# Optimization experiments

Hardware: AMD Instinct MI355X
Metric: run time of the kernel (lower is better)

Reference implementation:

```python
import jax, jax.numpy as jnp
import numpy as np

V, G, F, T = 500000, 25000, 256, 2


def setup_inputs() -> dict:
    key = jax.random.key(0)
    ks = jax.random.split(key, 10)
    s = 1.0 / np.sqrt(F)
    node_feats = jax.random.normal(ks[0], (V, F), jnp.float32)
    seg_ids = jnp.sort(jax.random.randint(ks[1], (V,), 0, G, dtype=jnp.int32))
    Wl = jax.random.uniform(ks[2], (T, 1, 2 * F), jnp.float32, -s, s)
    bl = jax.random.uniform(ks[3], (T, 1), jnp.float32, -s, s)
    Wp = jax.random.uniform(ks[4], (T, F, F), jnp.float32, -s, s)
    bp = jax.random.uniform(ks[5], (T, F), jnp.float32, -s, s)
    Wih = jax.random.uniform(ks[6], (T, 3 * F, F), jnp.float32, -s, s)
    Whh = jax.random.uniform(ks[7], (T, 3 * F, F), jnp.float32, -s, s)
    bih = jax.random.uniform(ks[8], (T, 3 * F), jnp.float32, -s, s)
    bhh = jax.random.uniform(ks[9], (T, 3 * F), jnp.float32, -s, s)
    return dict(node_feats=node_feats, seg_ids=seg_ids, Wl=Wl, bl=bl,
                Wp=Wp, bp=bp, Wih=Wih, Whh=Whh, bih=bih, bhh=bhh)


def _segment_softmax(z, seg):
    # z: (V,) per-node logits; softmax within each graph segment
    m = jax.ops.segment_max(z, seg, num_segments=G)
    m = jnp.where(jnp.isfinite(m), m, 0.0)  # guard empty segments
    e = jnp.exp(z - m[seg])
    d = jax.ops.segment_sum(e, seg, num_segments=G)
    return e / d[seg]


def _gru_cell(x, h, Wih, Whh, bih, bhh):
    # torch.nn.GRUCell semantics
    gi = x @ Wih.T + bih  # (G, 3F)
    gh = h @ Whh.T + bhh
    ir, iz, inn = jnp.split(gi, 3, axis=1)
    hr, hz, hn = jnp.split(gh, 3, axis=1)
    r = jax.nn.sigmoid(ir + hr)
    zg = jax.nn.sigmoid(iz + hz)
    n = jnp.tanh(inn + r * hn)
    return (1.0 - zg) * n + zg * h


def reference(node_feats, seg_ids, Wl, bl, Wp, bp, Wih, Whh, bih, bhh):
    # initial graph feats = sum of node feats per graph
    g_feats = jax.ops.segment_sum(node_feats, seg_ids, num_segments=G)  # (G, F)
    for t in range(T):
        ctx_in = jnp.concatenate([jax.nn.relu(g_feats)[seg_ids], node_feats], axis=1)  # (V, 2F)
        z = jax.nn.leaky_relu(ctx_in @ Wl[t].T + bl[t], 0.01)[:, 0]  # (V,)
        a = _segment_softmax(z, seg_ids)[:, None]  # (V, 1)
        hv = node_feats @ Wp[t].T + bp[t]  # dropout=0 -> identity
        g_repr = jax.ops.segment_sum(a * hv, seg_ids, num_segments=G)  # (G, F)
        context = jax.nn.elu(g_repr)
        g_feats = _gru_cell(context, g_feats, Wih[t], Whh[t], bih[t], bhh[t])
    return g_feats
```

## Files before the change

### kernel.cpp

```cpp
#include <hip/hip_runtime.h>
#include <cstdint>

typedef unsigned short u16;
typedef unsigned int u32;

#define V_N 500000
#define G_N 25000
#define F_N 256
#define GP_N 25088
#define CAP 64

typedef __attribute__((ext_vector_type(8))) __bf16 bf16x8;
typedef __attribute__((ext_vector_type(4))) float f32x4;

__device__ __forceinline__ u16 f2bf(float f) {
  u32 u = __builtin_bit_cast(u32, f);
  u += 0x7fffu + ((u >> 16) & 1u);
  return (u16)(u >> 16);
}
__device__ __forceinline__ float bf2f(u16 s) {
  u32 u = ((u32)s) << 16;
  return __builtin_bit_cast(float, u);
}
__device__ __forceinline__ float sigm(float x) { return 1.f / (1.f + __expf(-x)); }
__device__ __forceinline__ float tanh_fast(float x) {
  return 1.f - 2.f / (__expf(2.f * x) + 1.f);
}

__device__ __forceinline__ void load_lds16(const void* g, void* l) {
  __builtin_amdgcn_global_load_lds(
      (const __attribute__((address_space(1))) void*)g,
      (__attribute__((address_space(3))) void*)l, 16, 0, 0);
}

__global__ __launch_bounds__(256) void k_convw(const float* __restrict__ Wp,
                                               const float* __restrict__ Wih,
                                               const float* __restrict__ Whh,
                                               u16* __restrict__ Wpb, u16* __restrict__ W3) {
  int i = blockIdx.x * 256 + threadIdx.x;
  const int NP = 2 * F_N * F_N;
  if (i < NP) {
    Wpb[i] = f2bf(Wp[i]);
    return;
  }
  int j = i - NP;
  int t = j >> 19;
  int r = j & 524287;
  int row = r >> 9;
  int k = r & 511;
  int q = row >> 6;
  int gate = (row >> 4) & 3;
  int c = q * 16 + (row & 15);
  const float* wi = Wih + t * 196608;
  const float* wh = Whh + t * 196608;
  float v;
  if (gate == 0) {
    v = (k < 256) ? wi[c * 256 + k] : wh[c * 256 + (k - 256)];
  } else if (gate == 1) {
    v = (k < 256) ? wi[(256 + c) * 256 + k] : wh[(256 + c) * 256 + (k - 256)];
  } else if (gate == 2) {
    v = (k < 256) ? wi[(512 + c) * 256 + k] : 0.f;
  } else {
    v = (k >= 256) ? wh[(512 + c) * 256 + (k - 256)] : 0.f;
  }
  W3[j] = f2bf(v);
}

__global__ __launch_bounds__(256) void k_offsets(const int* __restrict__ seg, int* __restrict__ off) {
  int v = blockIdx.x * 256 + threadIdx.x;
  if (v > V_N) return;
  if (v == 0) {
    int c = seg[0];
    for (int g = 0; g <= c; ++g) off[g] = 0;
  } else if (v == V_N) {
    int pr = seg[V_N - 1];
    for (int g = pr + 1; g <= G_N; ++g) off[g] = V_N;
  } else {
    int pr = seg[v - 1], c = seg[v];
    for (int g = pr + 1; g <= c; ++g) off[g] = v;
  }
}

__device__ __forceinline__ float blk_sum(float v, float* lds4) {
#pragma unroll
  for (int m = 32; m >= 1; m >>= 1) v += __shfl_xor(v, m, 64);
  __syncthreads();
  if ((threadIdx.x & 63) == 0) lds4[threadIdx.x >> 6] = v;
  __syncthreads();
  return lds4[0] + lds4[1] + lds4[2] + lds4[3];
}
__device__ __forceinline__ float blk_max(float v, float* lds4) {
#pragma unroll
  for (int m = 32; m >= 1; m >>= 1) v = fmaxf(v, __shfl_xor(v, m, 64));
  __syncthreads();
  if ((threadIdx.x & 63) == 0) lds4[threadIdx.x >> 6] = v;
  __syncthreads();
  return fmaxf(fmaxf(lds4[0], lds4[1]), fmaxf(lds4[2], lds4[3]));
}

template <int USEXB>
__global__ __launch_bounds__(256) void k_node_fused(const float* __restrict__ nf,
                                                    const int* __restrict__ off,
                                                    const float* __restrict__ Wl,
                                                    const float* __restrict__ bl,
                                                    u16* __restrict__ xb,
                                                    float* __restrict__ q0, float* __restrict__ q1,
                                                    float* __restrict__ hbuf0, u16* __restrict__ x2a,
                                                    u16* __restrict__ x2b,
                                                    u16* __restrict__ sb, float* __restrict__ Ag) {
  int g = blockIdx.x;
  int tid = threadIdx.x, lane = tid & 63, w = tid >> 6;
  if (g >= G_N) {
    hbuf0[(size_t)g * F_N + tid] = 0.f;
    x2a[(size_t)g * 512 + 256 + tid] = 0;
    x2b[(size_t)g * 512 + 256 + tid] = 0;
    sb[(size_t)g * F_N + tid] = 0;
    if (tid == 0) Ag[g] = 0.f;
    return;
  }
  __shared__ __align__(16) u16 xcache[CAP * F_N];
  __shared__ float zrow[CAP];
  __shared__ float red[4][256];
  __shared__ float a_s[256];
  __shared__ float lds4[4];

  float w0[4], w1[4];
#pragma unroll
  for (int j = 0; j < 4; ++j) {
    w0[j] = Wl[256 + lane * 4 + j];
    w1[j] = Wl[512 + 256 + lane * 4 + j];
  }
  int s = off[g], e = off[g + 1];
  int n = e - s;
  float a0 = 0.f, a1 = 0.f, a2 = 0.f, a3 = 0.f;
  for (int v = s + w; v < e; v += 4) {
    const float4 x = *reinterpret_cast<const float4*>(nf + (size_t)v * F_N + lane * 4);
    a0 += x.x; a1 += x.y; a2 += x.z; a3 += x.w;
    uint2 pk;
    pk.x = (u32)f2bf(x.x) | ((u32)f2bf(x.y) << 16);
    pk.y = (u32)f2bf(x.z) | ((u32)f2bf(x.w) << 16);
    if (USEXB) *reinterpret_cast<uint2*>(xb + (size_t)v * F_N + lane * 4) = pk;
    int li = v - s;
    if (li < CAP) *reinterpret_cast<uint2*>(&xcache[li * F_N + lane * 4]) = pk;
    float d0 = x.x * w0[0] + x.y * w0[1] + x.z * w0[2] + x.w * w0[3];
    float d1 = x.x * w1[0] + x.y * w1[1] + x.z * w1[2] + x.w * w1[3];
#pragma unroll
    for (int m = 32; m >= 1; m >>= 1) {
      d0 += __shfl_xor(d0, m, 64);
      d1 += __shfl_xor(d1, m, 64);
    }
    if (lane == 0) {
      q0[v] = d0;
      q1[v] = d1;
      if (li < CAP) zrow[li] = d0;
    }
  }
  red[w][lane * 4 + 0] = a0;
  red[w][lane * 4 + 1] = a1;
  red[w][lane * 4 + 2] = a2;
  red[w][lane * 4 + 3] = a3;
  __threadfence_block();
  __syncthreads();
  float sval = red[0][tid] + red[1][tid] + red[2][tid] + red[3][tid];
  hbuf0[(size_t)g * F_N + tid] = sval;
  x2a[(size_t)g * 512 + 256 + tid] = f2bf(sval);

  float p = blk_sum(fmaxf(sval, 0.f) * Wl[tid], lds4) + bl[0];
  if (n == 0) {
    sb[(size_t)g * F_N + tid] = 0;
    if (tid == 0) Ag[g] = 0.f;
    return;
  }
  float mloc = -3.4e38f;
  for (int i = tid; i < n; i += 256) {
    float zq = (i < CAP) ? zrow[i] : q0[s + i];
    float z = p + zq;
    z = z >= 0.f ? z : 0.01f * z;
    mloc = fmaxf(mloc, z);
  }
  float mx = blk_max(mloc, lds4);
  float dloc = 0.f;
  for (int i = tid; i < n; i += 256) {
    float zq = (i < CAP) ? zrow[i] : q0[s + i];
    float z = p + zq;
    z = z >= 0.f ? z : 0.01f * z;
    dloc += __expf(z - mx);
  }
  float inv = 1.f / blk_sum(dloc, lds4);

  float acc4[4] = {0.f, 0.f, 0.f, 0.f};
  for (int c0 = 0; c0 < n; c0 += 256) {
    int cnt = min(256, n - c0);
    __syncthreads();
    if (tid < cnt) {
      int i = c0 + tid;
      float zq = (i < CAP) ? zrow[i] : q0[s + i];
      float z = p + zq;
      z = z >= 0.f ? z : 0.01f * z;
      a_s[tid] = __expf(z - mx) * inv;
    }
    __syncthreads();
    for (int j = w; j < cnt; j += 4) {
      int i = c0 + j;
      float a = a_s[j];
      uint2 u;
      if (i < CAP) {
        u = *reinterpret_cast<const uint2*>(&xcache[i * F_N + lane * 4]);
      } else if (USEXB) {
        u = *reinterpret_cast<const uint2*>(xb + (size_t)(s + i) * F_N + lane * 4);
      } else {
        float4 x = *reinterpret_cast<const float4*>(nf + (size_t)(s + i) * F_N + lane * 4);
        acc4[0] += a * x.x; acc4[1] += a * x.y; acc4[2] += a * x.z; acc4[3] += a * x.w;
        continue;
      }
      acc4[0] += a * bf2f((u16)(u.x & 0xffff));
      acc4[1] += a * bf2f((u16)(u.x >> 16));
      acc4[2] += a * bf2f((u16)(u.y & 0xffff));
      acc4[3] += a * bf2f((u16)(u.y >> 16));
    }
  }
  __syncthreads();
  red[w][lane * 4 + 0] = acc4[0];
  red[w][lane * 4 + 1] = acc4[1];
  red[w][lane * 4 + 2] = acc4[2];
  red[w][lane * 4 + 3] = acc4[3];
  __syncthreads();
  float sv = red[0][tid] + red[1][tid] + red[2][tid] + red[3][tid];
  sb[(size_t)g * F_N + tid] = f2bf(sv);
  if (tid == 0) Ag[g] = 1.f;
}

template <int USEXB>
__global__ __launch_bounds__(256) void k_attn(const float* __restrict__ h,
                                              const u16* __restrict__ xb, const float* __restrict__ nf,
                                              const float* __restrict__ q, const int* __restrict__ off,
                                              const float* __restrict__ Wl, const float* __restrict__ bl,
                                              int t, u16* __restrict__ sb, float* __restrict__ Ag) {
  int g = blockIdx.x;
  int tid = threadIdx.x, lane = tid & 63, w = tid >> 6;
  __shared__ float lds4[4];
  __shared__ float a_s[256];
  __shared__ float red[4][256];

  float hv = fmaxf(h[(size_t)g * F_N + tid], 0.f);
  float p = blk_sum(hv * Wl[t * 512 + tid], lds4) + bl[t];

  int s = off[g], n = off[g + 1] - s;
  if (n == 0) {
    sb[(size_t)g * F_N + tid] = 0;
    if (tid == 0) Ag[g] = 0.f;
    return;
  }
  float mloc = -3.4e38f;
  for (int i = tid; i < n; i += 256) {
    float z = p + q[s + i];
    z = z >= 0.f ? z : 0.01f * z;
    mloc = fmaxf(mloc, z);
  }
  float mx = blk_max(mloc, lds4);
  float dloc = 0.f;
  for (int i = tid; i < n; i += 256) {
    float z = p + q[s + i];
    z = z >= 0.f ? z : 0.01f * z;
    dloc += __expf(z - mx);
  }
  float inv = 1.f / blk_sum(dloc, lds4);

  float acc[4] = {0.f, 0.f, 0.f, 0.f};
  for (int c0 = 0; c0 < n; c0 += 256) {
    int cnt = min(256, n - c0);
    __syncthreads();
    if (tid < cnt) {
      float z = p + q[s + c0 + tid];
      z = z >= 0.f ? z : 0.01f * z;
      a_s[tid] = __expf(z - mx) * inv;
    }
    __syncthreads();
    for (int j = w; j < cnt; j += 4) {
      float a = a_s[j];
      size_t base = (size_t)(s + c0 + j) * F_N + lane * 4;
      if (USEXB) {
        uint2 u = *reinterpret_cast<const uint2*>(xb + base);
        acc[0] += a * bf2f((u16)(u.x & 0xffff));
        acc[1] += a * bf2f((u16)(u.x >> 16));
        acc[2] += a * bf2f((u16)(u.y & 0xffff));
        acc[3] += a * bf2f((u16)(u.y >> 16));
      } else {
        float4 x = *reinterpret_cast<const float4*>(nf + base);
        acc[0] += a * x.x; acc[1] += a * x.y; acc[2] += a * x.z; acc[3] += a * x.w;
      }
    }
  }
  __syncthreads();
  red[w][lane * 4 + 0] = acc[0];
  red[w][lane * 4 + 1] = acc[1];
  red[w][lane * 4 + 2] = acc[2];
  red[w][lane * 4 + 3] = acc[3];
  __syncthreads();
  float sv = red[0][tid] + red[1][tid] + red[2][tid] + red[3][tid];
  sb[(size_t)g * F_N + tid] = f2bf(sv);
  if (tid == 0) Ag[g] = 1.f;
}

__global__ __launch_bounds__(256) void k_gemm(const u16* __restrict__ A, const u16* __restrict__ B,
                                              int K, float* __restrict__ dst,
                                              u16* __restrict__ x2out, const float* __restrict__ AgH,
                                              const float* __restrict__ b1, const float* __restrict__ b2,
                                              int mode, int writehb) {
  __shared__ __align__(16) u16 As[128 * 64];
  __shared__ __align__(16) u16 Bs[128 * 64];
  int tid = threadIdx.x, lane = tid & 63, w = tid >> 6;
  int m0 = blockIdx.x * 128, n0 = blockIdx.y * 128;
  int wm = w >> 1, wn = w & 1;
  f32x4 zero = {0.f, 0.f, 0.f, 0.f};
  f32x4 acc[4][4];
#pragma unroll
  for (int i = 0; i < 4; ++i)
#pragma unroll
    for (int j = 0; j < 4; ++j) acc[i][j] = zero;

  int rowA = tid >> 3;
  int col8 = (tid & 7) * 8;
  for (int k0 = 0; k0 < K; k0 += 64) {
    __syncthreads();
#pragma unroll
    for (int c = 0; c < 4; ++c) {
      int r = c * 32 + rowA;
      const u16* gA = A + (size_t)(m0 + r) * K + k0 + col8;
      const u16* gB = B + (size_t)(n0 + r) * K + k0 + col8;
      char* lA = (char*)As + (c * 256 + w * 64) * 16;
      char* lB = (char*)Bs + (c * 256 + w * 64) * 16;
      load_lds16(gA, lA);
      load_lds16(gB, lB);
    }
    __syncthreads();
#pragma unroll
    for (int kk = 0; kk < 64; kk += 32) {
      bf16x8 af[4], bfr[4];
#pragma unroll
      for (int i = 0; i < 4; ++i) {
        af[i] = *reinterpret_cast<const bf16x8*>(&As[(wm * 64 + i * 16 + (lane & 15)) * 64 + kk + (lane >> 4) * 8]);
        bfr[i] = *reinterpret_cast<const bf16x8*>(&Bs[(wn * 64 + i * 16 + (lane & 15)) * 64 + kk + (lane >> 4) * 8]);
      }
#pragma unroll
      for (int i = 0; i < 4; ++i)
#pragma unroll
        for (int j = 0; j < 4; ++j)
          acc[i][j] = __builtin_amdgcn_mfma_f32_16x16x32_bf16(af[i], bfr[j], acc[i][j], 0, 0, 0);
    }
  }
  int crow0 = m0 + wm * 64 + (lane >> 4) * 4;
  if (mode == 1) {
    int ccol0 = n0 + wn * 64 + (lane & 15);
#pragma unroll
    for (int i = 0; i < 4; ++i)
#pragma unroll
      for (int j = 0; j < 4; ++j) {
        int col = ccol0 + j * 16;
#pragma unroll
        for (int r = 0; r < 4; ++r) {
          int row = crow0 + i * 16 + r;
          float v = acc[i][j][r] + AgH[row] * b1[col];
          v = v > 0.f ? v : (__expf(v) - 1.f);
          x2out[(size_t)row * 512 + col] = f2bf(v);
        }
      }
  } else {
    int qgrp = blockIdx.y * 2 + wn;
    int c = qgrp * 16 + (lane & 15);
    float bi0 = b1[c] + b2[c];
    float bi1 = b1[256 + c] + b2[256 + c];
    float bi2 = b1[512 + c];
    float bi3 = b2[512 + c];
#pragma unroll
    for (int i = 0; i < 4; ++i)
#pragma unroll
      for (int r = 0; r < 4; ++r) {
        int grow = crow0 + i * 16 + r;
        if (grow >= G_N) continue;
        float ir = acc[i][0][r] + bi0;
        float iz = acc[i][1][r] + bi1;
        float nn = acc[i][2][r] + bi2;
        float hn = acc[i][3][r] + bi3;
        float rg = sigm(ir);
        float zg = sigm(iz);
        float h0 = AgH[(size_t)grow * F_N + c];
        float nv = tanh_fast(nn + rg * hn);
        float hN = (1.f - zg) * nv + zg * h0;
        dst[(size_t)grow * F_N + c] = hN;
        if (writehb) x2out[(size_t)grow * 512 + 256 + c] = f2bf(hN);
      }
  }
}

extern "C" void kernel_launch(void* const* d_in, const int* in_sizes, int n_in,
                              void* d_out, int out_size, void* d_ws, size_t ws_size,
                              hipStream_t stream) {
  const float* nf = (const float*)d_in[0];
  const int* seg = (const int*)d_in[1];
  const float* Wl = (const float*)d_in[2];
  const float* bl = (const float*)d_in[3];
  const float* Wp = (const float*)d_in[4];
  const float* bp = (const float*)d_in[5];
  const float* Wih = (const float*)d_in[6];
  const float* Whh = (const float*)d_in[7];
  const float* bih = (const float*)d_in[8];
  const float* bhh = (const float*)d_in[9];
  float* out = (float*)d_out;

  char* p = (char*)d_ws;
  auto alloc = [&](size_t bytes) {
    char* r = p;
    p += (bytes + 511) & ~(size_t)511;
    return r;
  };
  float* q0 = (float*)alloc((size_t)V_N * 4);
  float* q1 = (float*)alloc((size_t)V_N * 4);
  int* off = (int*)alloc((size_t)(G_N + 1) * 4);
  float* hbuf0 = (float*)alloc((size_t)GP_N * F_N * 4);
  float* hbuf1 = (float*)alloc((size_t)GP_N * F_N * 4);
  u16* sb = (u16*)alloc((size_t)GP_N * F_N * 2);
  float* Ag = (float*)alloc((size_t)GP_N * 4);
  u16* X2a = (u16*)alloc((size_t)GP_N * 512 * 2);
  u16* X2b = (u16*)alloc((size_t)GP_N * 512 * 2);
  u16* Wpb = (u16*)alloc((size_t)2 * F_N * F_N * 2);
  u16* W3 = (u16*)alloc((size_t)2 * 1024 * 512 * 2);
  size_t fixed = (size_t)(p - (char*)d_ws);
  bool usexb = (fixed + (size_t)V_N * F_N * 2) <= ws_size;
  u16* xb = usexb ? (u16*)alloc((size_t)V_N * F_N * 2) : nullptr;

  k_convw<<<4608, 256, 0, stream>>>(Wp, Wih, Whh, Wpb, W3);
  k_offsets<<<(V_N + 1 + 255) / 256, 256, 0, stream>>>(seg, off);
  if (usexb)
    k_node_fused<1><<<GP_N, 256, 0, stream>>>(nf, off, Wl, bl, xb, q0, q1, hbuf0, X2a, X2b, sb, Ag);
  else
    k_node_fused<0><<<GP_N, 256, 0, stream>>>(nf, off, Wl, bl, xb, q0, q1, hbuf0, X2a, X2b, sb, Ag);

  k_gemm<<<dim3(GP_N / 128, 2), 256, 0, stream>>>(sb, Wpb, 256,
                                                  nullptr, X2a, Ag, bp, nullptr, 1, 0);
  k_gemm<<<dim3(GP_N / 128, 8), 256, 0, stream>>>(X2a, W3, 512,
                                                  hbuf1, X2b, hbuf0,
                                                  bih, bhh, 2, 1);
  if (usexb)
    k_attn<1><<<G_N, 256, 0, stream>>>(hbuf1, xb, nf, q1, off, Wl, bl, 1, sb, Ag);
  else
    k_attn<0><<<G_N, 256, 0, stream>>>(hbuf1, xb, nf, q1, off, Wl, bl, 1, sb, Ag);
  k_gemm<<<dim3(GP_N / 128, 2), 256, 0, stream>>>(sb, Wpb + 65536, 256,
                                                  nullptr, X2b, Ag, bp + 256, nullptr, 1, 0);
  k_gemm<<<dim3(GP_N / 128, 8), 256, 0, stream>>>(X2b, W3 + 524288, 512,
                                                  out, nullptr, hbuf1,
                                                  bih + 768, bhh + 768, 2, 0);
}
```

Measured before the change: 520.7 us.

## Map one graph per wavefront and split fused node kernel from attention

The per-graph node and attention kernels now assign one graph per 64-lane wavefront, with four graphs per block, instead of one graph per 256-thread block. This drops the LDS reductions and __syncthreads barriers. The fused node kernel is split: k_node computes sums, bf16 copies and q projections, and the first-step attention becomes a separate k_attn launch. The LDS node cache and the fp32 fallback path are removed, and the attention loop reads 16-byte bf16 rows with two rows per wavefront step. The intent is to cut synchronization overhead and raise occupancy for small segments of about 20 nodes. The cost is an extra launch, a re-read of xb for step 0, and an unconditional xb allocation that assumes the workspace is large enough.

```diff
diff --git a/kernel.cpp b/kernel.cpp
--- a/kernel.cpp
+++ b/kernel.cpp
@@ -8,7 +8,6 @@
 #define G_N 25000
 #define F_N 256
 #define GP_N 25088
-#define CAP 64
 
 typedef __attribute__((ext_vector_type(8))) __bf16 bf16x8;
 typedef __attribute__((ext_vector_type(4))) float f32x4;
@@ -26,6 +25,7 @@
 __device__ __forceinline__ float tanh_fast(float x) {
   return 1.f - 2.f / (__expf(2.f * x) + 1.f);
 }
+__device__ __forceinline__ float lrelu(float z) { return z >= 0.f ? z : 0.01f * z; }
 
 __device__ __forceinline__ void load_lds16(const void* g, void* l) {
   __builtin_amdgcn_global_load_lds(
@@ -81,69 +81,40 @@
   }
 }
 
-__device__ __forceinline__ float blk_sum(float v, float* lds4) {
-#pragma unroll
-  for (int m = 32; m >= 1; m >>= 1) v += __shfl_xor(v, m, 64);
-  __syncthreads();
-  if ((threadIdx.x & 63) == 0) lds4[threadIdx.x >> 6] = v;
-  __syncthreads();
-  return lds4[0] + lds4[1] + lds4[2] + lds4[3];
-}
-__device__ __forceinline__ float blk_max(float v, float* lds4) {
-#pragma unroll
-  for (int m = 32; m >= 1; m >>= 1) v = fmaxf(v, __shfl_xor(v, m, 64));
-  __syncthreads();
-  if ((threadIdx.x & 63) == 0) lds4[threadIdx.x >> 6] = v;
-  __syncthreads();
-  return fmaxf(fmaxf(lds4[0], lds4[1]), fmaxf(lds4[2], lds4[3]));
-}
-
-template <int USEXB>
-__global__ __launch_bounds__(256) void k_node_fused(const float* __restrict__ nf,
-                                                    const int* __restrict__ off,
-                                                    const float* __restrict__ Wl,
-                                                    const float* __restrict__ bl,
-                                                    u16* __restrict__ xb,
-                                                    float* __restrict__ q0, float* __restrict__ q1,
-                                                    float* __restrict__ hbuf0, u16* __restrict__ x2a,
-                                                    u16* __restrict__ x2b,
-                                                    u16* __restrict__ sb, float* __restrict__ Ag) {
-  int g = blockIdx.x;
-  int tid = threadIdx.x, lane = tid & 63, w = tid >> 6;
+__global__ __launch_bounds__(256) void k_node(const float* __restrict__ nf,
+                                              const int* __restrict__ off,
+                                              const float* __restrict__ Wl,
+                                              u16* __restrict__ xb,
+                                              float* __restrict__ q0, float* __restrict__ q1,
+                                              float* __restrict__ hbuf0, u16* __restrict__ x2a,
+                                              u16* __restrict__ x2b,
+                                              u16* __restrict__ sb, float* __restrict__ Ag) {
+  int g = blockIdx.x * 4 + (threadIdx.x >> 6);
+  int lane = threadIdx.x & 63;
+  if (g >= GP_N) return;
   if (g >= G_N) {
-    hbuf0[(size_t)g * F_N + tid] = 0.f;
-    x2a[(size_t)g * 512 + 256 + tid] = 0;
-    x2b[(size_t)g * 512 + 256 + tid] = 0;
-    sb[(size_t)g * F_N + tid] = 0;
-    if (tid == 0) Ag[g] = 0.f;
+    float4 z4 = {0.f, 0.f, 0.f, 0.f};
+    uint2 z2 = {0u, 0u};
+    *reinterpret_cast<float4*>(hbuf0 + (size_t)g * F_N + lane * 4) = z4;
+    *reinterpret_cast<uint2*>(x2a + (size_t)g * 512 + 256 + lane * 4) = z2;
+    *reinterpret_cast<uint2*>(x2b + (size_t)g * 512 + 256 + lane * 4) = z2;
+    *reinterpret_cast<uint2*>(sb + (size_t)g * F_N + lane * 4) = z2;
+    if (lane == 0) Ag[g] = 0.f;
     return;
   }
-  __shared__ __align__(16) u16 xcache[CAP * F_N];
-  __shared__ float zrow[CAP];
-  __shared__ float red[4][256];
-  __shared__ float a_s[256];
-  __shared__ float lds4[4];
-
-  float w0[4], w1[4];
-#pragma unroll
-  for (int j = 0; j < 4; ++j) {
-    w0[j] = Wl[256 + lane * 4 + j];
-    w1[j] = Wl[512 + 256 + lane * 4 + j];
-  }
+  const float4 w0 = *reinterpret_cast<const float4*>(Wl + 256 + lane * 4);
+  const float4 w1 = *reinterpret_cast<const float4*>(Wl + 768 + lane * 4);
   int s = off[g], e = off[g + 1];
-  int n = e - s;
   float a0 = 0.f, a1 = 0.f, a2 = 0.f, a3 = 0.f;
-  for (int v = s + w; v < e; v += 4) {
+  for (int v = s; v < e; ++v) {
     const float4 x = *reinterpret_cast<const float4*>(nf + (size_t)v * F_N + lane * 4);
     a0 += x.x; a1 += x.y; a2 += x.z; a3 += x.w;
     uint2 pk;
     pk.x = (u32)f2bf(x.x) | ((u32)f2bf(x.y) << 16);
     pk.y = (u32)f2bf(x.z) | ((u32)f2bf(x.w) << 16);
-    if (USEXB) *reinterpret_cast<uint2*>(xb + (size_t)v * F_N + lane * 4) = pk;
-    int li = v - s;
-    if (li < CAP) *reinterpret_cast<uint2*>(&xcache[li * F_N + lane * 4]) = pk;
-    float d0 = x.x * w0[0] + x.y * w0[1] + x.z * w0[2] + x.w * w0[3];
-    float d1 = x.x * w1[0] + x.y * w1[1] + x.z * w1[2] + x.w * w1[3];
+    *reinterpret_cast<uint2*>(xb + (size_t)v * F_N + lane * 4) = pk;
+    float d0 = x.x * w0.x + x.y * w0.y + x.z * w0.z + x.w * w0.w;
+    float d1 = x.x * w1.x + x.y * w1.y + x.z * w1.z + x.w * w1.w;
 #pragma unroll
     for (int m = 32; m >= 1; m >>= 1) {
       d0 += __shfl_xor(d0, m, 64);
@@ -152,154 +123,87 @@
     if (lane == 0) {
       q0[v] = d0;
       q1[v] = d1;
-      if (li < CAP) zrow[li] = d0;
-    }
-  }
-  red[w][lane * 4 + 0] = a0;
-  red[w][lane * 4 + 1] = a1;
-  red[w][lane * 4 + 2] = a2;
-  red[w][lane * 4 + 3] = a3;
-  __threadfence_block();
-  __syncthreads();
-  float sval = red[0][tid] + red[1][tid] + red[2][tid] + red[3][tid];
-  hbuf0[(size_t)g * F_N + tid] = sval;
-  x2a[(size_t)g * 512 + 256 + tid] = f2bf(sval);
-
-  float p = blk_sum(fmaxf(sval, 0.f) * Wl[tid], lds4) + bl[0];
-  if (n == 0) {
-    sb[(size_t)g * F_N + tid] = 0;
-    if (tid == 0) Ag[g] = 0.f;
-    return;
-  }
-  float mloc = -3.4e38f;
-  for (int i = tid; i < n; i += 256) {
-    float zq = (i < CAP) ? zrow[i] : q0[s + i];
-    float z = p + zq;
-    z = z >= 0.f ? z : 0.01f * z;
-    mloc = fmaxf(mloc, z);
-  }
-  float mx = blk_max(mloc, lds4);
-  float dloc = 0.f;
-  for (int i = tid; i < n; i += 256) {
-    float zq = (i < CAP) ? zrow[i] : q0[s + i];
-    float z = p + zq;
-    z = z >= 0.f ? z : 0.01f * z;
-    dloc += __expf(z - mx);
-  }
-  float inv = 1.f / blk_sum(dloc, lds4);
-
-  float acc4[4] = {0.f, 0.f, 0.f, 0.f};
-  for (int c0 = 0; c0 < n; c0 += 256) {
-    int cnt = min(256, n - c0);
-    __syncthreads();
-    if (tid < cnt) {
-      int i = c0 + tid;
-      float zq = (i < CAP) ? zrow[i] : q0[s + i];
-      float z = p + zq;
-      z = z >= 0.f ? z : 0.01f * z;
-      a_s[tid] = __expf(z - mx) * inv;
-    }
-    __syncthreads();
-    for (int j = w; j < cnt; j += 4) {
-      int i = c0 + j;
-      float a = a_s[j];
-      uint2 u;
-      if (i < CAP) {
-        u = *reinterpret_cast<const uint2*>(&xcache[i * F_N + lane * 4]);
-      } else if (USEXB) {
-        u = *reinterpret_cast<const uint2*>(xb + (size_t)(s + i) * F_N + lane * 4);
-      } else {
-        float4 x = *reinterpret_cast<const float4*>(nf + (size_t)(s + i) * F_N + lane * 4);
-        acc4[0] += a * x.x; acc4[1] += a * x.y; acc4[2] += a * x.z; acc4[3] += a * x.w;
-        continue;
-      }
-      acc4[0] += a * bf2f((u16)(u.x & 0xffff));
-      acc4[1] += a * bf2f((u16)(u.x >> 16));
-      acc4[2] += a * bf2f((u16)(u.y & 0xffff));
-      acc4[3] += a * bf2f((u16)(u.y >> 16));
-    }
-  }
-  __syncthreads();
-  red[w][lane * 4 + 0] = acc4[0];
-  red[w][lane * 4 + 1] = acc4[1];
-  red[w][lane * 4 + 2] = acc4[2];
-  red[w][lane * 4 + 3] = acc4[3];
-  __syncthreads();
-  float sv = red[0][tid] + red[1][tid] + red[2][tid] + red[3][tid];
-  sb[(size_t)g * F_N + tid] = f2bf(sv);
-  if (tid == 0) Ag[g] = 1.f;
-}
-
-template <int USEXB>
+    }
+  }
+  float4 h4 = {a0, a1, a2, a3};
+  *reinterpret_cast<float4*>(hbuf0 + (size_t)g * F_N + lane * 4) = h4;
+  uint2 hs;
+  hs.x = (u32)f2bf(a0) | ((u32)f2bf(a1) << 16);
+  hs.y = (u32)f2bf(a2) | ((u32)f2bf(a3) << 16);
+  *reinterpret_cast<uint2*>(x2a + (size_t)g * 512 + 256 + lane * 4) = hs;
+}
+
 __global__ __launch_bounds__(256) void k_attn(const float* __restrict__ h,
-                                              const u16* __restrict__ xb, const float* __restrict__ nf,
-                                              const float* __restrict__ q, const int* __restrict__ off,
-                                              const float* __restrict__ Wl, const float* __restrict__ bl,
-                                              int t, u16* __restrict__ sb, float* __restrict__ Ag) {
-  int g = blockIdx.x;
-  int tid = threadIdx.x, lane = tid & 63, w = tid >> 6;
-  __shared__ float lds4[4];
-  __shared__ float a_s[256];
-  __shared__ float red[4][256];
-
-  float hv = fmaxf(h[(size_t)g * F_N + tid], 0.f);
-  float p = blk_sum(hv * Wl[t * 512 + tid], lds4) + bl[t];
+                                              const u16* __restrict__ xb,
+                                              const float* __restrict__ q,
+                                              const int* __restrict__ off,
+                                              const float* __restrict__ Wl,
+                                              const float* __restrict__ bl, int t,
+                                              u16* __restrict__ sb, float* __restrict__ Ag) {
+  int g = blockIdx.x * 4 + (threadIdx.x >> 6);
+  int lane = threadIdx.x & 63;
+  if (g >= G_N) return;
+
+  const float4 hv = *reinterpret_cast<const float4*>(h + (size_t)g * F_N + lane * 4);
+  const float4 wv = *reinterpret_cast<const float4*>(Wl + t * 512 + lane * 4);
+  float pd = fmaxf(hv.x, 0.f) * wv.x + fmaxf(hv.y, 0.f) * wv.y +
+             fmaxf(hv.z, 0.f) * wv.z + fmaxf(hv.w, 0.f) * wv.w;
+#pragma unroll
+  for (int m = 32; m >= 1; m >>= 1) pd += __shfl_xor(pd, m, 64);
+  float p = pd + bl[t];
 
   int s = off[g], n = off[g + 1] - s;
   if (n == 0) {
-    sb[(size_t)g * F_N + tid] = 0;
-    if (tid == 0) Ag[g] = 0.f;
+    if (lane < 32) {
+      uint4 z = {0u, 0u, 0u, 0u};
+      *reinterpret_cast<uint4*>(sb + (size_t)g * F_N + lane * 8) = z;
+    }
+    if (lane == 0) Ag[g] = 0.f;
     return;
   }
   float mloc = -3.4e38f;
-  for (int i = tid; i < n; i += 256) {
-    float z = p + q[s + i];
-    z = z >= 0.f ? z : 0.01f * z;
-    mloc = fmaxf(mloc, z);
-  }
-  float mx = blk_max(mloc, lds4);
+  for (int i = lane; i < n; i += 64) mloc = fmaxf(mloc, lrelu(p + q[s + i]));
+#pragma unroll
+  for (int m = 32; m >= 1; m >>= 1) mloc = fmaxf(mloc, __shfl_xor(mloc, m, 64));
+  float mx = mloc;
   float dloc = 0.f;
-  for (int i = tid; i < n; i += 256) {
-    float z = p + q[s + i];
-    z = z >= 0.f ? z : 0.01f * z;
-    dloc += __expf(z - mx);
-  }
-  float inv = 1.f / blk_sum(dloc, lds4);
-
-  float acc[4] = {0.f, 0.f, 0.f, 0.f};
-  for (int c0 = 0; c0 < n; c0 += 256) {
-    int cnt = min(256, n - c0);
-    __syncthreads();
-    if (tid < cnt) {
-      float z = p + q[s + c0 + tid];
-      z = z >= 0.f ? z : 0.01f * z;
-      a_s[tid] = __expf(z - mx) * inv;
-    }
-    __syncthreads();
-    for (int j = w; j < cnt; j += 4) {
-      float a = a_s[j];
-      size_t base = (size_t)(s + c0 + j) * F_N + lane * 4;
-      if (USEXB) {
-        uint2 u = *reinterpret_cast<const uint2*>(xb + base);
-        acc[0] += a * bf2f((u16)(u.x & 0xffff));
-        acc[1] += a * bf2f((u16)(u.x >> 16));
-        acc[2] += a * bf2f((u16)(u.y & 0xffff));
-        acc[3] += a * bf2f((u16)(u.y >> 16));
-      } else {
-        float4 x = *reinterpret_cast<const float4*>(nf + base);
-        acc[0] += a * x.x; acc[1] += a * x.y; acc[2] += a * x.z; acc[3] += a * x.w;
-      }
-    }
-  }
-  __syncthreads();
-  red[w][lane * 4 + 0] = acc[0];
-  red[w][lane * 4 + 1] = acc[1];
-  red[w][lane * 4 + 2] = acc[2];
-  red[w][lane * 4 + 3] = acc[3];
-  __syncthreads();
-  float sv = red[0][tid] + red[1][tid] + red[2][tid] + red[3][tid];
-  sb[(size_t)g * F_N + tid] = f2bf(sv);
-  if (tid == 0) Ag[g] = 1.f;
+  for (int i = lane; i < n; i += 64) dloc += __expf(lrelu(p + q[s + i]) - mx);
+#pragma unroll
+  for (int m = 32; m >= 1; m >>= 1) dloc += __shfl_xor(dloc, m, 64);
+  float inv = 1.f / dloc;
+
+  int half = lane >> 5;
+  int cl = (lane & 31) * 8;
+  float acc[8] = {0.f, 0.f, 0.f, 0.f, 0.f, 0.f, 0.f, 0.f};
+  for (int i = 0; i < n; i += 2) {
+    int r = i + half;
+    float a = 0.f;
+    int row = s;
+    if (r < n) {
+      a = __expf(lrelu(p + q[s + r]) - mx) * inv;
+      row = s + r;
+    }
+    uint4 x = *reinterpret_cast<const uint4*>(xb + (size_t)row * F_N + cl);
+    acc[0] += a * bf2f((u16)(x.x & 0xffff));
+    acc[1] += a * bf2f((u16)(x.x >> 16));
+    acc[2] += a * bf2f((u16)(x.y & 0xffff));
+    acc[3] += a * bf2f((u16)(x.y >> 16));
+    acc[4] += a * bf2f((u16)(x.z & 0xffff));
+    acc[5] += a * bf2f((u16)(x.z >> 16));
+    acc[6] += a * bf2f((u16)(x.w & 0xffff));
+    acc[7] += a * bf2f((u16)(x.w >> 16));
+  }
+#pragma unroll
+  for (int k = 0; k < 8; ++k) acc[k] += __shfl_xor(acc[k], 32, 64);
+  if (lane < 32) {
+    uint4 o;
+    o.x = (u32)f2bf(acc[0]) | ((u32)f2bf(acc[1]) << 16);
+    o.y = (u32)f2bf(acc[2]) | ((u32)f2bf(acc[3]) << 16);
+    o.z = (u32)f2bf(acc[4]) | ((u32)f2bf(acc[5]) << 16);
+    o.w = (u32)f2bf(acc[6]) | ((u32)f2bf(acc[7]) << 16);
+    *reinterpret_cast<uint4*>(sb + (size_t)g * F_N + cl) = o;
+  }
+  if (lane == 0) Ag[g] = 1.f;
 }
 
 __global__ __launch_bounds__(256) void k_gemm(const u16* __restrict__ A, const u16* __restrict__ B,
@@ -425,29 +329,20 @@
   u16* X2b = (u16*)alloc((size_t)GP_N * 512 * 2);
   u16* Wpb = (u16*)alloc((size_t)2 * F_N * F_N * 2);
   u16* W3 = (u16*)alloc((size_t)2 * 1024 * 512 * 2);
-  size_t fixed = (size_t)(p - (char*)d_ws);
-  bool usexb = (fixed + (size_t)V_N * F_N * 2) <= ws_size;
-  u16* xb = usexb ? (u16*)alloc((size_t)V_N * F_N * 2) : nullptr;
+  u16* xb = (u16*)alloc((size_t)V_N * F_N * 2);
 
   k_convw<<<4608, 256, 0, stream>>>(Wp, Wih, Whh, Wpb, W3);
   k_offsets<<<(V_N + 1 + 255) / 256, 256, 0, stream>>>(seg, off);
-  if (usexb)
-    k_node_fused<1><<<GP_N, 256, 0, stream>>>(nf, off, Wl, bl, xb, q0, q1, hbuf0, X2a, X2b, sb, Ag);
-  else
-    k_node_fused<0><<<GP_N, 256, 0, stream>>>(nf, off, Wl, bl, xb, q0, q1, hbuf0, X2a, X2b, sb, Ag);
-
+  k_node<<<GP_N / 4, 256, 0, stream>>>(nf, off, Wl, xb, q0, q1, hbuf0, X2a, X2b, sb, Ag);
+
+  k_attn<<<G_N / 4, 256, 0, stream>>>(hbuf0, xb, q0, off, Wl, bl, 0, sb, Ag);
   k_gemm<<<dim3(GP_N / 128, 2), 256, 0, stream>>>(sb, Wpb, 256,
                                                   nullptr, X2a, Ag, bp, nullptr, 1, 0);
   k_gemm<<<dim3(GP_N / 128, 8), 256, 0, stream>>>(X2a, W3, 512,
-                                                  hbuf1, X2b, hbuf0,
-                                                  bih, bhh, 2, 1);
-  if (usexb)
-    k_attn<1><<<G_N, 256, 0, stream>>>(hbuf1, xb, nf, q1, off, Wl, bl, 1, sb, Ag);
-  else
-    k_attn<0><<<G_N, 256, 0, stream>>>(hbuf1, xb, nf, q1, off, Wl, bl, 1, sb, Ag);
+                                                  hbuf1, X2b, hbuf0, bih, bhh, 2, 1);
+  k_attn<<<G_N / 4, 256, 0, stream>>>(hbuf1, xb, q1, off, Wl, bl, 1, sb, Ag);
   k_gemm<<<dim3(GP_N / 128, 2), 256, 0, stream>>>(sb, Wpb + 65536, 256,
                                                   nullptr, X2b, Ag, bp + 256, nullptr, 1, 0);
   k_gemm<<<dim3(GP_N / 128, 8), 256, 0, stream>>>(X2b, W3 + 524288, 512,
-                                                  out, nullptr, hbuf1,
-                                                  bih + 768, bhh + 768, 2, 0);
-}
+                                                  out, nullptr, hbuf1, bih + 768, bhh + 768, 2, 0);
+}
```

Measured after the change: 510.8 us. No clear change (-1.9%).
